# Performance work log

Hardware: AMD Instinct MI355X
Metric: run time of the kernel (lower is better)

The kernel has to match this reference:

```python
import jax, jax.numpy as jnp
import numpy as np
from jax import lax

N_WAY, N_SUPPORT, N_QUERY = 16, 256, 512
D_IN, D_EMB = 4096, 1024
N_CLUSTERS, MAX_ITER = 5, 100


def setup_inputs() -> dict:
    key = jax.random.key(0)
    k1, k2, kw, kb = jax.random.split(key, 4)
    support = jax.random.normal(k1, (N_WAY, N_SUPPORT, D_IN), jnp.float32)
    query = jax.random.normal(k2, (N_WAY, N_QUERY, D_IN), jnp.float32)
    W = jax.random.normal(kw, (D_IN, D_EMB), jnp.float32) / np.float32(np.sqrt(D_IN))
    b = jax.random.normal(kb, (D_EMB,), jnp.float32) * 0.01
    return {"support": support, "query": query, "W": W, "b": b}


def _sqdist(x, c):
    # x [n,d], c [k,d] -> [n,k] squared euclidean distances
    return (jnp.sum(x * x, -1, keepdims=True)
            - 2.0 * (x @ c.T)
            + jnp.sum(c * c, -1))


def _kmeans(x, init):
    # x [n,d], init [k,d]; fixed-iteration Lloyd's kmeans (converged state is a
    # fixed point of the update, matching the torch early-break semantics).
    n = x.shape[0]
    ones = jnp.ones((n,), x.dtype)

    def step(c, _):
        assign = jnp.argmin(_sqdist(x, c), axis=1)              # [n]
        sums = jax.ops.segment_sum(x, assign, num_segments=N_CLUSTERS)
        cnt = jax.ops.segment_sum(ones, assign, num_segments=N_CLUSTERS)
        # empty cluster keeps its old centroid
        new_c = jnp.where(cnt[:, None] > 0,
                          sums / jnp.maximum(cnt, 1.0)[:, None], c)
        return new_c, None

    c, _ = lax.scan(step, init, None, length=MAX_ITER)
    return c


def _forward(support, query, W, b):
    # encoder: shared linear over flattened (n_way * n) rows
    s = (support.reshape(-1, D_IN) @ W + b).reshape(N_WAY, N_SUPPORT, D_EMB)
    q = (query.reshape(-1, D_IN) @ W + b).reshape(N_WAY, N_QUERY, D_EMB)

    # per-class kmeans init: random subset of that class's support embeddings
    keys = jax.random.split(jax.random.key(42), N_WAY)

    def init_fn(key, class_emb):
        idx = jax.random.permutation(key, N_SUPPORT)[:N_CLUSTERS]
        return class_emb[idx]

    inits = jax.vmap(init_fn)(keys, s)                 # [n_way, k, d]
    cluster_protos = jax.vmap(_kmeans)(s, inits)       # [n_way, k, d]
    class_protos = cluster_protos.mean(axis=1)         # [n_way, d]

    # cdist(query_emb [b,n,d], protos [c,d]) -> [b,n,c]
    d2 = (jnp.sum(q * q, -1)[..., None]
          - 2.0 * jnp.einsum('bnd,cd->bnc', q, class_protos)
          + jnp.sum(class_protos * class_protos, -1))
    distances = jnp.sqrt(jnp.maximum(d2, 0.0))
    return -distances                                  # logits [n_way, n_query, n_classes]


def reference(support, query, W, b):
    return _forward(support, query, W, b)
```

## Files before the change

### kernel.cpp

```cpp
#include <hip/hip_runtime.h>
#include <cstdint>
#include <cstddef>


typedef __attribute__((ext_vector_type(4))) float f32x4;
typedef __attribute__((ext_vector_type(8))) short s16x8;
typedef __attribute__((ext_vector_type(4))) short s16x4;
typedef __attribute__((ext_vector_type(8))) __bf16 bf16x8;

__device__ __forceinline__ unsigned short f2bf(float f) {
  unsigned u = __float_as_uint(f);
  return (unsigned short)((u + 0x7FFFu + ((u >> 16) & 1u)) >> 16);
}
__device__ __forceinline__ float bf2f(unsigned short h) {
  return __uint_as_float(((unsigned)h) << 16);
}

typedef const __attribute__((address_space(1))) void GV;
typedef __attribute__((address_space(3))) void LV;
__device__ __forceinline__ void gload_lds16(const void* g, void* l) {
  __builtin_amdgcn_global_load_lds((GV*)g, (LV*)l, 16, 0, 0);
}
__device__ __forceinline__ f32x4 mfma16(bf16x8 a, bf16x8 b, f32x4 c) {
  return __builtin_amdgcn_mfma_f32_16x16x32_bf16(a, b, c, 0, 0, 0);
}
__device__ __forceinline__ float wave_sum(float v) {
#pragma unroll
  for (int st = 1; st < 64; st <<= 1) v += __shfl_xor(v, st);
  return v;
}

__device__ __forceinline__ void tf2x32(unsigned k0, unsigned k1, unsigned x0,
                                       unsigned x1, unsigned& y0, unsigned& y1) {
  unsigned ks0 = k0, ks1 = k1, ks2 = k0 ^ k1 ^ 0x1BD11BDAu;
  x0 += ks0; x1 += ks1;
  const int rA[4] = {13, 15, 26, 6};
  const int rB[4] = {17, 29, 16, 24};
#define ROTL(v, d) (((v) << (d)) | ((v) >> (32 - (d))))
#define RG(R)                                     \
  _Pragma("unroll") for (int i = 0; i < 4; i++) { \
    x0 += x1; x1 = ROTL(x1, R[i]); x1 ^= x0;      \
  }
  RG(rA); x0 += ks1; x1 += ks2 + 1u;
  RG(rB); x0 += ks2; x1 += ks0 + 2u;
  RG(rA); x0 += ks0; x1 += ks1 + 3u;
  RG(rB); x0 += ks1; x1 += ks2 + 4u;
  RG(rA); x0 += ks2; x1 += ks0 + 5u;
#undef RG
#undef ROTL
  y0 = x0; y1 = x1;
}

__global__ __launch_bounds__(256) void prep_k(
    const float* __restrict__ W, const float* __restrict__ sup,
    const float* __restrict__ qry, short* __restrict__ WhiT,
    short* __restrict__ WloT, short* __restrict__ Shi,
    short* __restrict__ Slo, short* __restrict__ Qhi) {
  __shared__ float tile[64][65];
  int t = threadIdx.x;
  if (blockIdx.x < 1024) {
    int bk = blockIdx.x & 63, bn = blockIdx.x >> 6;
#pragma unroll
    for (int i = 0; i < 4; i++) {
      int row = i * 16 + (t >> 4);
      int col = (t & 15) * 4;
      f32x4 v =
          *(const f32x4*)(W + (size_t)(bk * 64 + row) * 1024 + bn * 64 + col);
      tile[row][col + 0] = v[0]; tile[row][col + 1] = v[1];
      tile[row][col + 2] = v[2]; tile[row][col + 3] = v[3];
    }
    __syncthreads();
#pragma unroll
    for (int i = 0; i < 4; i++) {
      int nrow = i * 16 + (t >> 4);
      int kcol = (t & 15) * 4;
      s16x4 hv, lv;
#pragma unroll
      for (int e = 0; e < 4; e++) {
        float v = tile[kcol + e][nrow];
        unsigned short h = f2bf(v);
        hv[e] = (short)h;
        lv[e] = (short)f2bf(v - bf2f(h));
      }
      size_t off = (size_t)(bn * 64 + nrow) * 4096 + bk * 64 + kcol;
      *(s16x4*)(WhiT + off) = hv;
      *(s16x4*)(WloT + off) = lv;
    }
  } else {
    size_t gid = (size_t)(blockIdx.x - 1024) * 256 + t;
    const size_t sup_n8 = (size_t)4096 * 4096 / 8;
    if (gid < sup_n8) {
      const float* src = sup + gid * 8;
      f32x4 v0 = *(const f32x4*)src, v1 = *(const f32x4*)(src + 4);
      s16x8 h, l;
#pragma unroll
      for (int e = 0; e < 4; e++) {
        unsigned short hh = f2bf(v0[e]);
        h[e] = (short)hh; l[e] = (short)f2bf(v0[e] - bf2f(hh));
      }
#pragma unroll
      for (int e = 0; e < 4; e++) {
        unsigned short hh = f2bf(v1[e]);
        h[4 + e] = (short)hh; l[4 + e] = (short)f2bf(v1[e] - bf2f(hh));
      }
      *(s16x8*)(Shi + gid * 8) = h;
      *(s16x8*)(Slo + gid * 8) = l;
    } else {
      size_t q = gid - sup_n8;
      const float* src = qry + q * 8;
      f32x4 v0 = *(const f32x4*)src, v1 = *(const f32x4*)(src + 4);
      s16x8 h;
#pragma unroll
      for (int e = 0; e < 4; e++) h[e] = (short)f2bf(v0[e]);
#pragma unroll
      for (int e = 0; e < 4; e++) h[4 + e] = (short)f2bf(v1[e]);
      *(s16x8*)(Qhi + q * 8) = h;
    }
  }
}

__global__ __launch_bounds__(256) void gemm_sup_k(
    const short* __restrict__ Shi, const short* __restrict__ Slo,
    const short* __restrict__ WhiT, const short* __restrict__ WloT,
    const float* __restrict__ bias, float* __restrict__ emb) {
  __shared__ short lds[24576];
  short* Ah = lds;
  short* Al = lds + 4096;
  short* Bh = lds + 8192;
  short* Bl = lds + 16384;
  const int bid = blockIdx.x;
  const int bm = bid & 63, bn = bid >> 6;
  const int t = threadIdx.x, lane = t & 63, w = t >> 6;
  const int wr = w >> 1, wc = w & 1;
  const int fr = lane & 15, kg = lane >> 4;
  const int ls = lane >> 3, lc = lane & 7;
  const short* Ag = Shi + (size_t)bm * 64 * 4096;
  const short* Alg = Slo + (size_t)bm * 64 * 4096;
  f32x4 acc[2][4] = {};

  for (int kt = 0; kt < 64; ++kt) {
    const int k0 = kt * 64;
    __syncthreads();
    const int cch = (lc ^ ls) * 8;
#pragma unroll
    for (int j = 0; j < 2; j++) {
      int rowl = w * 16 + j * 8 + ls;
      size_t aoff = (size_t)rowl * 4096 + k0 + cch;
      int ldst = (w * 16 + j * 8) * 64;
      gload_lds16(Ag + aoff, Ah + ldst);
      gload_lds16(Alg + aoff, Al + ldst);
    }
#pragma unroll
    for (int j = 0; j < 4; j++) {
      int rowl = w * 32 + j * 8 + ls;
      size_t boff = (size_t)(bn * 128 + rowl) * 4096 + k0 + cch;
      int ldst = (w * 32 + j * 8) * 64;
      gload_lds16(WhiT + boff, Bh + ldst);
      gload_lds16(WloT + boff, Bl + ldst);
    }
    __syncthreads();
#pragma unroll
    for (int ks = 0; ks < 2; ++ks) {
      const int cx = ((ks * 4 + kg) ^ (fr & 7)) * 8;
      bf16x8 ahf[2], alf[2], bhf[4], blf[4];
#pragma unroll
      for (int mi = 0; mi < 2; mi++) {
        int arow = wr * 32 + mi * 16 + fr;
        ahf[mi] = __builtin_bit_cast(bf16x8, *(const s16x8*)(Ah + arow * 64 + cx));
        alf[mi] = __builtin_bit_cast(bf16x8, *(const s16x8*)(Al + arow * 64 + cx));
      }
#pragma unroll
      for (int ni = 0; ni < 4; ni++) {
        int brow = wc * 64 + ni * 16 + fr;
        bhf[ni] = __builtin_bit_cast(bf16x8, *(const s16x8*)(Bh + brow * 64 + cx));
        blf[ni] = __builtin_bit_cast(bf16x8, *(const s16x8*)(Bl + brow * 64 + cx));
      }
#pragma unroll
      for (int mi = 0; mi < 2; mi++)
#pragma unroll
        for (int ni = 0; ni < 4; ni++) {
          acc[mi][ni] = mfma16(ahf[mi], bhf[ni], acc[mi][ni]);
          acc[mi][ni] = mfma16(ahf[mi], blf[ni], acc[mi][ni]);
          acc[mi][ni] = mfma16(alf[mi], bhf[ni], acc[mi][ni]);
        }
    }
  }
#pragma unroll
  for (int ni = 0; ni < 4; ni++) {
    int gc = bn * 128 + wc * 64 + ni * 16 + fr;
    float bv = bias[gc];
#pragma unroll
    for (int mi = 0; mi < 2; mi++) {
      int gr = bm * 64 + wr * 32 + mi * 16 + kg * 4;
#pragma unroll
      for (int r = 0; r < 4; r++)
        emb[(size_t)(gr + r) * 1024 + gc] = acc[mi][ni][r] + bv;
    }
  }
}

__global__ __launch_bounds__(256) void gemm_qry_k(
    const short* __restrict__ Qhi, const short* __restrict__ WhiT,
    const float* __restrict__ bias, float* __restrict__ emb) {
  __shared__ short lds[16384];
  short* Ah = lds;
  short* Bh = lds + 8192;
  const int bid = blockIdx.x;
  const int bm = bid & 63, bn = bid >> 6;
  const int t = threadIdx.x, lane = t & 63, w = t >> 6;
  const int wr = w >> 1, wc = w & 1;
  const int fr = lane & 15, kg = lane >> 4;
  const int ls = lane >> 3, lc = lane & 7;
  const short* Ag = Qhi + (size_t)bm * 128 * 4096;
  f32x4 acc[4][4] = {};

  for (int kt = 0; kt < 64; ++kt) {
    const int k0 = kt * 64;
    __syncthreads();
    const int cch = (lc ^ ls) * 8;
#pragma unroll
    for (int j = 0; j < 4; j++) {
      int rowl = w * 32 + j * 8 + ls;
      size_t aoff = (size_t)rowl * 4096 + k0 + cch;
      size_t boff = (size_t)(bn * 128 + rowl) * 4096 + k0 + cch;
      int ldst = (w * 32 + j * 8) * 64;
      gload_lds16(Ag + aoff, Ah + ldst);
      gload_lds16(WhiT + boff, Bh + ldst);
    }
    __syncthreads();
#pragma unroll
    for (int ks = 0; ks < 2; ++ks) {
      const int cx = ((ks * 4 + kg) ^ (fr & 7)) * 8;
      bf16x8 ahf[4], bhf[4];
#pragma unroll
      for (int mi = 0; mi < 4; mi++) {
        int arow = wr * 64 + mi * 16 + fr;
        ahf[mi] = __builtin_bit_cast(bf16x8, *(const s16x8*)(Ah + arow * 64 + cx));
      }
#pragma unroll
      for (int ni = 0; ni < 4; ni++) {
        int brow = wc * 64 + ni * 16 + fr;
        bhf[ni] = __builtin_bit_cast(bf16x8, *(const s16x8*)(Bh + brow * 64 + cx));
      }
#pragma unroll
      for (int mi = 0; mi < 4; mi++)
#pragma unroll
        for (int ni = 0; ni < 4; ni++)
          acc[mi][ni] = mfma16(ahf[mi], bhf[ni], acc[mi][ni]);
    }
  }
#pragma unroll
  for (int ni = 0; ni < 4; ni++) {
    int gc = bn * 128 + wc * 64 + ni * 16 + fr;
    float bv = bias[gc];
#pragma unroll
    for (int mi = 0; mi < 4; mi++) {
      int gr = 4096 + bm * 128 + wr * 64 + mi * 16 + kg * 4;
#pragma unroll
      for (int r = 0; r < 4; r++)
        emb[(size_t)(gr + r) * 1024 + gc] = acc[mi][ni][r] + bv;
    }
  }
}

__global__ __launch_bounds__(256) void gemm_all_k(
    const float* __restrict__ sup, const float* __restrict__ qry,
    const short* __restrict__ WhiT, const short* __restrict__ WloT,
    const float* __restrict__ bias, float* __restrict__ emb) {
  __shared__ short lds[4 * 128 * 64];
  short* Ah = lds;
  short* Al = lds + 8192;
  short* Bh = lds + 16384;
  short* Bl = lds + 24576;
  const int bid = blockIdx.x;
  const int bm = bid % 96, bn = bid / 96;
  const bool is_sup = bm < 32;
  const int t = threadIdx.x, lane = t & 63, w = t >> 6;
  const int wr = w >> 1, wc = w & 1;
  const int fr = lane & 15, kg = lane >> 4;
  const float* Abase = is_sup ? (sup + (size_t)bm * 128 * 4096)
                              : (qry + (size_t)(bm - 32) * 128 * 4096);
  f32x4 acc[4][4] = {};
  const int ls = lane >> 3, lc = lane & 7;

  for (int kt = 0; kt < 64; ++kt) {
    const int k0 = kt * 64;
    __syncthreads();
#pragma unroll
    for (int i = 0; i < 4; i++) {
      int row = i * 32 + w * 8 + ls;
      const float* src = Abase + (size_t)row * 4096 + k0 + lc * 8;
      f32x4 v0 = *(const f32x4*)src;
      f32x4 v1 = *(const f32x4*)(src + 4);
      s16x8 hs;
#pragma unroll
      for (int e = 0; e < 4; e++) hs[e] = (short)f2bf(v0[e]);
#pragma unroll
      for (int e = 0; e < 4; e++) hs[4 + e] = (short)f2bf(v1[e]);
      int chunk = lc ^ (row & 7);
      *(s16x8*)(Ah + row * 64 + chunk * 8) = hs;
      if (is_sup) {
        s16x8 lsv;
#pragma unroll
        for (int e = 0; e < 4; e++)
          lsv[e] = (short)f2bf(v0[e] - bf2f((unsigned short)hs[e]));
#pragma unroll
        for (int e = 0; e < 4; e++)
          lsv[4 + e] = (short)f2bf(v1[e] - bf2f((unsigned short)hs[4 + e]));
        *(s16x8*)(Al + row * 64 + chunk * 8) = lsv;
      }
    }
#pragma unroll
    for (int j = 0; j < 4; j++) {
      int rowl = w * 32 + j * 8 + ls;
      int cch = (lc ^ (ls & 7)) * 8;
      size_t goff = (size_t)(bn * 128 + rowl) * 4096 + k0 + cch;
      gload_lds16(WhiT + goff, Bh + (w * 32 + j * 8) * 64);
      if (is_sup) gload_lds16(WloT + goff, Bl + (w * 32 + j * 8) * 64);
    }
    __syncthreads();
#pragma unroll
    for (int ks = 0; ks < 2; ++ks) {
      const int cx = ((ks * 4 + kg) ^ (fr & 7)) * 8;
      bf16x8 ahf[4], bhf[4];
#pragma unroll
      for (int mi = 0; mi < 4; mi++) {
        int arow = wr * 64 + mi * 16 + fr;
        ahf[mi] = __builtin_bit_cast(bf16x8, *(const s16x8*)(Ah + arow * 64 + cx));
      }
#pragma unroll
      for (int ni = 0; ni < 4; ni++) {
        int brow = wc * 64 + ni * 16 + fr;
        bhf[ni] = __builtin_bit_cast(bf16x8, *(const s16x8*)(Bh + brow * 64 + cx));
      }
      if (is_sup) {
        bf16x8 alf[4], blf[4];
#pragma unroll
        for (int mi = 0; mi < 4; mi++) {
          int arow = wr * 64 + mi * 16 + fr;
          alf[mi] =
              __builtin_bit_cast(bf16x8, *(const s16x8*)(Al + arow * 64 + cx));
        }
#pragma unroll
        for (int ni = 0; ni < 4; ni++) {
          int brow = wc * 64 + ni * 16 + fr;
          blf[ni] =
              __builtin_bit_cast(bf16x8, *(const s16x8*)(Bl + brow * 64 + cx));
        }
#pragma unroll
        for (int mi = 0; mi < 4; mi++)
#pragma unroll
          for (int ni = 0; ni < 4; ni++) {
            acc[mi][ni] = mfma16(ahf[mi], bhf[ni], acc[mi][ni]);
            acc[mi][ni] = mfma16(ahf[mi], blf[ni], acc[mi][ni]);
            acc[mi][ni] = mfma16(alf[mi], bhf[ni], acc[mi][ni]);
          }
      } else {
#pragma unroll
        for (int mi = 0; mi < 4; mi++)
#pragma unroll
          for (int ni = 0; ni < 4; ni++)
            acc[mi][ni] = mfma16(ahf[mi], bhf[ni], acc[mi][ni]);
      }
    }
  }
#pragma unroll
  for (int ni = 0; ni < 4; ni++) {
    int gc = bn * 128 + wc * 64 + ni * 16 + fr;
    float bv = bias[gc];
#pragma unroll
    for (int mi = 0; mi < 4; mi++) {
      int gr = bm * 128 + wr * 64 + mi * 16 + kg * 4;
#pragma unroll
      for (int r = 0; r < 4; r++)
        emb[(size_t)(gr + r) * 1024 + gc] = acc[mi][ni][r] + bv;
    }
  }
}

__global__ __launch_bounds__(256) void gram_k(const float* __restrict__ emb,
                                              float* __restrict__ G) {
  int c = blockIdx.x >> 4, tl = blockIdx.x & 15, ti = tl >> 2, tj = tl & 3;
  __shared__ float As[64][36];
  __shared__ float Bs[32][68];
  int t = threadIdx.x, ty = t >> 4, tx = t & 15;
  const float* base = emb + (size_t)c * 256 * 1024;
  float acc[4][4] = {};
  for (int k0 = 0; k0 < 1024; k0 += 32) {
    __syncthreads();
    {
      int r = t >> 2, seg = t & 3;
      const float* pa = base + (size_t)(ti * 64 + r) * 1024 + k0 + seg * 8;
      f32x4 va0 = *(const f32x4*)pa, va1 = *(const f32x4*)(pa + 4);
      *(f32x4*)(&As[r][seg * 8]) = va0;
      *(f32x4*)(&As[r][seg * 8 + 4]) = va1;
      const float* pb = base + (size_t)(tj * 64 + r) * 1024 + k0 + seg * 8;
      f32x4 vb0 = *(const f32x4*)pb, vb1 = *(const f32x4*)(pb + 4);
#pragma unroll
      for (int e = 0; e < 4; e++) Bs[seg * 8 + e][r] = vb0[e];
#pragma unroll
      for (int e = 0; e < 4; e++) Bs[seg * 8 + 4 + e][r] = vb1[e];
    }
    __syncthreads();
#pragma unroll 4
    for (int kk = 0; kk < 32; kk++) {
      float a0 = As[ty * 4 + 0][kk], a1 = As[ty * 4 + 1][kk];
      float a2 = As[ty * 4 + 2][kk], a3 = As[ty * 4 + 3][kk];
      f32x4 bv = *(const f32x4*)(&Bs[kk][tx * 4]);
#pragma unroll
      for (int jdx = 0; jdx < 4; jdx++) {
        acc[0][jdx] = fmaf(a0, bv[jdx], acc[0][jdx]);
        acc[1][jdx] = fmaf(a1, bv[jdx], acc[1][jdx]);
        acc[2][jdx] = fmaf(a2, bv[jdx], acc[2][jdx]);
        acc[3][jdx] = fmaf(a3, bv[jdx], acc[3][jdx]);
      }
    }
  }
#pragma unroll
  for (int i = 0; i < 4; i++) {
    int gr = ti * 64 + ty * 4 + i;
#pragma unroll
    for (int j = 0; j < 4; j++)
      G[(size_t)c * 65536 + (size_t)gr * 256 + tj * 64 + tx * 4 + j] = acc[i][j];
  }
}

__global__ __launch_bounds__(256) void diag_k(const float* __restrict__ emb,
                                              float* __restrict__ G) {
  int r = blockIdx.x * 4 + (threadIdx.x >> 6);
  int lane = threadIdx.x & 63;
  const float* x = emb + (size_t)r * 1024;
  double acc = 0.0;
#pragma unroll
  for (int ch = 0; ch < 16; ch++) {
    float v = x[ch * 64 + lane];
    acc = fma((double)v, (double)v, acc);
  }
#pragma unroll
  for (int st = 1; st < 64; st <<= 1) acc += __shfl_xor(acc, st);
  if (lane == 0) {
    int c = r >> 8, i = r & 255;
    G[(size_t)c * 65536 + (size_t)i * 256 + i] = (float)acc;
  }
}

__global__ __launch_bounds__(256) void kmeans2_k(const float* __restrict__ G,
                                                 float* __restrict__ wts) {
  const int c = blockIdx.x;
  const int t = threadIdx.x, lane = t & 63, w = t >> 6;
  __shared__ unsigned dmL[256], nmL[256];
  __shared__ unsigned short chg[256];
  __shared__ unsigned sk[256];
  __shared__ unsigned idx5[5];
  __shared__ float Tpart[4][5], Tu[5], C2[5], Minv[5];
  __shared__ int Hp[4][5], Ncnt[5], cntW[4];

  {
    unsigned o0, o1, s0k, s1k, y0, y1;
    tf2x32(0u, 42u, 0u, (unsigned)c, o0, o1);
    tf2x32(o0, o1, 0u, 1u, s0k, s1k);
    tf2x32(s0k, s1k, 0u, (unsigned)t, y0, y1);
    sk[t] = y0 ^ y1;
  }
  __syncthreads();
  {
    unsigned kt_ = sk[t];
    int rank = 0;
    for (int j = 0; j < 256; j++) {
      unsigned kj = sk[j];
      rank += (kj < kt_ || (kj == kt_ && j < t)) ? 1 : 0;
    }
    if (rank < 5) idx5[rank] = (unsigned)t;
  }
  if (t < 5) Minv[t] = 1.0f;
  __syncthreads();

  unsigned m = 0;
#pragma unroll
  for (int k = 0; k < 5; k++) m |= (idx5[k] == (unsigned)t) ? (1u << k) : 0u;

  const float* Gc = G + (size_t)c * 65536;
  float s0 = Gc[(size_t)idx5[0] * 256 + t];
  float s1 = Gc[(size_t)idx5[1] * 256 + t];
  float s2 = Gc[(size_t)idx5[2] * 256 + t];
  float s3 = Gc[(size_t)idx5[3] * 256 + t];
  float s4 = Gc[(size_t)idx5[4] * 256 + t];

  for (int it = 0; it < 100; ++it) {
    float v0 = (m & 1u) ? s0 : 0.0f;
    float v1 = (m & 2u) ? s1 : 0.0f;
    float v2 = (m & 4u) ? s2 : 0.0f;
    float v3 = (m & 8u) ? s3 : 0.0f;
    float v4 = (m & 16u) ? s4 : 0.0f;
#pragma unroll
    for (int st = 1; st < 64; st <<= 1) {
      v0 += __shfl_xor(v0, st); v1 += __shfl_xor(v1, st);
      v2 += __shfl_xor(v2, st); v3 += __shfl_xor(v3, st);
      v4 += __shfl_xor(v4, st);
    }
    if (lane == 0) {
      Tpart[w][0] = v0; Tpart[w][1] = v1; Tpart[w][2] = v2;
      Tpart[w][3] = v3; Tpart[w][4] = v4;
    }
    __syncthreads();
    if (t < 5) {
      float T = Tpart[0][t] + Tpart[1][t] + Tpart[2][t] + Tpart[3][t];
      float iv = Minv[t];
      Tu[t] = T * iv * iv;
      C2[t] = -2.0f * iv;
    }
    __syncthreads();
    float d0 = fmaf(C2[0], s0, Tu[0]);
    float d1 = fmaf(C2[1], s1, Tu[1]);
    float d2 = fmaf(C2[2], s2, Tu[2]);
    float d3 = fmaf(C2[3], s3, Tu[3]);
    float d4 = fmaf(C2[4], s4, Tu[4]);
    int a_t = 0;
    float dmn = d0;
    if (d1 < dmn) { dmn = d1; a_t = 1; }
    if (d2 < dmn) { dmn = d2; a_t = 2; }
    if (d3 < dmn) { dmn = d3; a_t = 3; }
    if (d4 < dmn) { dmn = d4; a_t = 4; }
#pragma unroll
    for (int k = 0; k < 5; k++) {
      unsigned long long bal = __ballot(a_t == k);
      if (lane == 0) Hp[w][k] = (int)__popcll(bal);
    }
    __syncthreads();
    if (t < 5) Ncnt[t] = Hp[0][t] + Hp[1][t] + Hp[2][t] + Hp[3][t];
    __syncthreads();
    unsigned nm = 0;
#pragma unroll
    for (int k = 0; k < 5; k++) {
      int bit = (Ncnt[k] > 0) ? (a_t == k ? 1 : 0) : (int)((m >> k) & 1u);
      nm |= ((unsigned)bit) << k;
    }
    unsigned dmb = nm ^ m;
    unsigned long long bal = __ballot(dmb != 0);
    int myrank = (int)__popcll(bal & ((1ull << lane) - 1ull));
    if (lane == 0) cntW[w] = (int)__popcll(bal);
    nmL[t] = nm; dmL[t] = dmb;
    __syncthreads();
    int base = 0, ntot = 0;
#pragma unroll
    for (int ww = 0; ww < 4; ww++) {
      int cw = cntW[ww];
      if (ww < w) base += cw;
      ntot += cw;
    }
    if (ntot == 0) break;
    if (dmb != 0) chg[base + myrank] = (unsigned short)t;
    m = nm;
    if (t < 5 && Ncnt[t] > 0) Minv[t] = 1.0f / (float)Ncnt[t];
    __syncthreads();
    for (int p = 0; p < ntot; p += 4) {
      float g[4]; int jj[4];
#pragma unroll
      for (int q = 0; q < 4; q++) {
        int idx = p + q;
        jj[q] = (idx < ntot) ? (int)chg[idx] : -1;
        g[q] = (jj[q] >= 0) ? Gc[(size_t)jj[q] * 256 + t] : 0.0f;
      }
#pragma unroll
      for (int q = 0; q < 4; q++) {
        if (jj[q] < 0) continue;
        unsigned db = dmL[jj[q]], nb = nmL[jj[q]];
        float gv = g[q];
        if (db & 1u)  s0 += (nb & 1u)  ? gv : -gv;
        if (db & 2u)  s1 += (nb & 2u)  ? gv : -gv;
        if (db & 4u)  s2 += (nb & 4u)  ? gv : -gv;
        if (db & 8u)  s3 += (nb & 8u)  ? gv : -gv;
        if (db & 16u) s4 += (nb & 16u) ? gv : -gv;
      }
    }
    __syncthreads();
  }
  float wv = 0.0f;
#pragma unroll
  for (int k = 0; k < 5; k++)
    if ((m >> k) & 1u) wv += 0.2f * Minv[k];
  wts[c * 256 + t] = wv;
}

__global__ __launch_bounds__(256) void proto1_k(const float* __restrict__ emb,
                                                const float* __restrict__ wts,
                                                float* __restrict__ part) {
  int c = blockIdx.x & 15, seg = blockIdx.x >> 4, t = threadIdx.x;
  __shared__ float wl[16];
  if (t < 16) wl[t] = wts[c * 256 + seg * 16 + t];
  __syncthreads();
  f32x4 acc = {};
  const float* base = emb + (size_t)(c * 256 + seg * 16) * 1024 + t * 4;
#pragma unroll
  for (int j = 0; j < 16; j++) {
    f32x4 v = *(const f32x4*)(base + (size_t)j * 1024);
    float wj = wl[j];
#pragma unroll
    for (int e = 0; e < 4; e++) acc[e] = fmaf(wj, v[e], acc[e]);
  }
  *(f32x4*)(part + ((size_t)seg * 16 + c) * 1024 + t * 4) = acc;
}

__global__ __launch_bounds__(256) void proto2_k(const float* __restrict__ part,
                                                float* __restrict__ protos) {
  int c = blockIdx.x, t = threadIdx.x;
  f32x4 acc = {};
#pragma unroll
  for (int seg = 0; seg < 16; seg++) {
    f32x4 v = *(const f32x4*)(part + ((size_t)seg * 16 + c) * 1024 + t * 4);
#pragma unroll
    for (int e = 0; e < 4; e++) acc[e] += v[e];
  }
  *(f32x4*)(protos + (size_t)c * 1024 + t * 4) = acc;
}

__global__ __launch_bounds__(256) void proto_k(const float* __restrict__ emb,
                                               const float* __restrict__ wts,
                                               float* __restrict__ protos) {
  int c = blockIdx.x, t = threadIdx.x;
  __shared__ float wl[256];
  wl[t] = wts[c * 256 + t];
  __syncthreads();
  f32x4 acc = {};
  const float* base = emb + (size_t)c * 256 * 1024 + t * 4;
  for (int j = 0; j < 256; j++) {
    f32x4 v = *(const f32x4*)(base + (size_t)j * 1024);
    float wj = wl[j];
#pragma unroll
    for (int e = 0; e < 4; e++) acc[e] = fmaf(wj, v[e], acc[e]);
  }
  *(f32x4*)(protos + (size_t)c * 1024 + t * 4) = acc;
}

__global__ __launch_bounds__(256) void dist_k(const float* __restrict__ emb,
                                              const float* __restrict__ protos,
                                              float* __restrict__ out) {
  __shared__ float P[16 * 1024];
  int t = threadIdx.x, lane = t & 63, w = t >> 6;
#pragma unroll
  for (int i = 0; i < 16; i++) {
    int off = i * 1024 + t * 4;
    *(f32x4*)(P + off) = *(const f32x4*)(protos + off);
  }
  __syncthreads();
  float psq_keep = 0.0f;
  for (int p = 0; p < 16; p++) {
    float partial = 0.0f;
#pragma unroll
    for (int ch = 0; ch < 16; ch++) {
      float x = P[p * 1024 + ch * 64 + lane];
      partial = fmaf(x, x, partial);
    }
    partial = wave_sum(partial);
    if (lane == p) psq_keep = partial;
  }
  const float* qbase = emb + (size_t)4096 * 1024;
  int r0 = blockIdx.x * 16 + w * 4;
  for (int ri = 0; ri < 4; ri++) {
    int row = r0 + ri;
    const float* q = qbase + (size_t)row * 1024;
    float qv[16];
#pragma unroll
    for (int ch = 0; ch < 16; ch++) qv[ch] = q[ch * 64 + lane];
    float qsq = 0.0f;
#pragma unroll
    for (int ch = 0; ch < 16; ch++) qsq = fmaf(qv[ch], qv[ch], qsq);
    qsq = wave_sum(qsq);
    float dsel = 0.0f;
    for (int p = 0; p < 16; p++) {
      float dp = 0.0f;
#pragma unroll
      for (int ch = 0; ch < 16; ch++)
        dp = fmaf(qv[ch], P[p * 1024 + ch * 64 + lane], dp);
      dp = wave_sum(dp);
      if (lane == p) dsel = dp;
    }
    if (lane < 16) {
      float d2 = qsq - 2.0f * dsel + psq_keep;
      d2 = fmaxf(d2, 0.0f);
      out[(size_t)row * 16 + lane] = -sqrtf(d2);
    }
  }
}

extern "C" void kernel_launch(void* const* d_in, const int* in_sizes, int n_in,
                              void* d_out, int out_size, void* d_ws,
                              size_t ws_size, hipStream_t stream) {
  const float* sup = (const float*)d_in[0];
  const float* qry = (const float*)d_in[1];
  const float* W = (const float*)d_in[2];
  const float* b = (const float*)d_in[3];
  float* out = (float*)d_out;
  char* ws = (char*)d_ws;
  (void)in_sizes; (void)n_in; (void)out_size;

  const size_t NEED_FAST = 206651392ULL;
  if (ws_size >= NEED_FAST) {
    short* WhiT = (short*)(ws + 0);
    short* WloT = (short*)(ws + 8388608);
    short* Shi = (short*)(ws + 16777216);
    short* Slo = (short*)(ws + 50331648);
    short* Qhi = (short*)(ws + 83886080);
    float* emb = (float*)(ws + 150994944);
    float* G = (float*)(ws + 201326592);
    float* wts = (float*)(ws + 205520896);
    float* protos = (float*)(ws + 205537280);
    float* part = (float*)(ws + 205602816);

    prep_k<<<25600, 256, 0, stream>>>(W, sup, qry, WhiT, WloT, Shi, Slo, Qhi);
    gemm_sup_k<<<512, 256, 0, stream>>>(Shi, Slo, WhiT, WloT, b, emb);
    gemm_qry_k<<<512, 256, 0, stream>>>(Qhi, WhiT, b, emb);
    gram_k<<<256, 256, 0, stream>>>(emb, G);
    diag_k<<<1024, 256, 0, stream>>>(emb, G);
    kmeans2_k<<<16, 256, 0, stream>>>(G, wts);
    proto1_k<<<256, 256, 0, stream>>>(emb, wts, part);
    proto2_k<<<16, 256, 0, stream>>>(part, protos);
    dist_k<<<512, 256, 0, stream>>>(emb, protos, out);
  } else {
    short* WhiT = (short*)(ws + 0);
    short* WloT = (short*)(ws + 8388608);
    float* emb = (float*)(ws + 16777216);
    float* G = (float*)(ws + 67108864);
    float* wts = (float*)(ws + 71303168);
    float* protos = (float*)(ws + 71319552);

    prep_k<<<1024, 256, 0, stream>>>(W, sup, qry, WhiT, WloT, (short*)0,
                                     (short*)0, (short*)0);
    gemm_all_k<<<768, 256, 0, stream>>>(sup, qry, WhiT, WloT, b, emb);
    gram_k<<<256, 256, 0, stream>>>(emb, G);
    diag_k<<<1024, 256, 0, stream>>>(emb, G);
    kmeans2_k<<<16, 256, 0, stream>>>(G, wts);
    proto_k<<<16, 256, 0, stream>>>(emb, wts, protos);
    dist_k<<<512, 256, 0, stream>>>(emb, protos, out);
  }
}
```

Baseline: 444.0 us.

## Run kmeans in a single wavefront, fuse gram and diag, grid-stride prep

The kmeans kernel moves from 256 threads (4 waves) to one 64-lane wavefront per class. Each lane holds 4 points, so all block barriers and LDS exchanges are replaced by wave shuffles and ballots. The initial random selection becomes an iterative shuffle min-reduction instead of an O(n) rank count per thread. Gram and diagonal computation are fused into one launch, with the gram blocks skipping diagonal writes to avoid a race, and prep becomes grid-stride with far fewer blocks. The aim is to cut the serial 100-iteration kmeans latency dominated by __syncthreads and to save launch overhead, at the cost of more per-lane work and register pressure.

```diff
diff --git a/kernel.cpp b/kernel.cpp
--- a/kernel.cpp
+++ b/kernel.cpp
@@ -87,34 +87,38 @@
       *(s16x4*)(WloT + off) = lv;
     }
   } else {
-    size_t gid = (size_t)(blockIdx.x - 1024) * 256 + t;
     const size_t sup_n8 = (size_t)4096 * 4096 / 8;
-    if (gid < sup_n8) {
-      const float* src = sup + gid * 8;
-      f32x4 v0 = *(const f32x4*)src, v1 = *(const f32x4*)(src + 4);
-      s16x8 h, l;
-#pragma unroll
-      for (int e = 0; e < 4; e++) {
-        unsigned short hh = f2bf(v0[e]);
-        h[e] = (short)hh; l[e] = (short)f2bf(v0[e] - bf2f(hh));
-      }
-#pragma unroll
-      for (int e = 0; e < 4; e++) {
-        unsigned short hh = f2bf(v1[e]);
-        h[4 + e] = (short)hh; l[4 + e] = (short)f2bf(v1[e] - bf2f(hh));
-      }
-      *(s16x8*)(Shi + gid * 8) = h;
-      *(s16x8*)(Slo + gid * 8) = l;
-    } else {
-      size_t q = gid - sup_n8;
-      const float* src = qry + q * 8;
-      f32x4 v0 = *(const f32x4*)src, v1 = *(const f32x4*)(src + 4);
-      s16x8 h;
-#pragma unroll
-      for (int e = 0; e < 4; e++) h[e] = (short)f2bf(v0[e]);
-#pragma unroll
-      for (int e = 0; e < 4; e++) h[4 + e] = (short)f2bf(v1[e]);
-      *(s16x8*)(Qhi + q * 8) = h;
+    const size_t tot_n8 = sup_n8 + (size_t)8192 * 4096 / 8;
+    size_t stride = (size_t)(gridDim.x - 1024) * 256;
+    for (size_t gid = (size_t)(blockIdx.x - 1024) * 256 + t; gid < tot_n8;
+         gid += stride) {
+      if (gid < sup_n8) {
+        const float* src = sup + gid * 8;
+        f32x4 v0 = *(const f32x4*)src, v1 = *(const f32x4*)(src + 4);
+        s16x8 h, l;
+#pragma unroll
+        for (int e = 0; e < 4; e++) {
+          unsigned short hh = f2bf(v0[e]);
+          h[e] = (short)hh; l[e] = (short)f2bf(v0[e] - bf2f(hh));
+        }
+#pragma unroll
+        for (int e = 0; e < 4; e++) {
+          unsigned short hh = f2bf(v1[e]);
+          h[4 + e] = (short)hh; l[4 + e] = (short)f2bf(v1[e] - bf2f(hh));
+        }
+        *(s16x8*)(Shi + gid * 8) = h;
+        *(s16x8*)(Slo + gid * 8) = l;
+      } else {
+        size_t q = gid - sup_n8;
+        const float* src = qry + q * 8;
+        f32x4 v0 = *(const f32x4*)src, v1 = *(const f32x4*)(src + 4);
+        s16x8 h;
+#pragma unroll
+        for (int e = 0; e < 4; e++) h[e] = (short)f2bf(v0[e]);
+#pragma unroll
+        for (int e = 0; e < 4; e++) h[4 + e] = (short)f2bf(v1[e]);
+        *(s16x8*)(Qhi + q * 8) = h;
+      }
     }
   }
 }
@@ -378,208 +382,231 @@
   }
 }
 
-__global__ __launch_bounds__(256) void gram_k(const float* __restrict__ emb,
-                                              float* __restrict__ G) {
-  int c = blockIdx.x >> 4, tl = blockIdx.x & 15, ti = tl >> 2, tj = tl & 3;
-  __shared__ float As[64][36];
-  __shared__ float Bs[32][68];
-  int t = threadIdx.x, ty = t >> 4, tx = t & 15;
-  const float* base = emb + (size_t)c * 256 * 1024;
-  float acc[4][4] = {};
-  for (int k0 = 0; k0 < 1024; k0 += 32) {
-    __syncthreads();
-    {
-      int r = t >> 2, seg = t & 3;
-      const float* pa = base + (size_t)(ti * 64 + r) * 1024 + k0 + seg * 8;
-      f32x4 va0 = *(const f32x4*)pa, va1 = *(const f32x4*)(pa + 4);
-      *(f32x4*)(&As[r][seg * 8]) = va0;
-      *(f32x4*)(&As[r][seg * 8 + 4]) = va1;
-      const float* pb = base + (size_t)(tj * 64 + r) * 1024 + k0 + seg * 8;
-      f32x4 vb0 = *(const f32x4*)pb, vb1 = *(const f32x4*)(pb + 4);
-#pragma unroll
-      for (int e = 0; e < 4; e++) Bs[seg * 8 + e][r] = vb0[e];
-#pragma unroll
-      for (int e = 0; e < 4; e++) Bs[seg * 8 + 4 + e][r] = vb1[e];
-    }
-    __syncthreads();
+__global__ __launch_bounds__(256) void gramdiag_k(const float* __restrict__ emb,
+                                                  float* __restrict__ G) {
+  if (blockIdx.x < 256) {
+    int c = blockIdx.x >> 4, tl = blockIdx.x & 15, ti = tl >> 2, tj = tl & 3;
+    __shared__ float As[64][36];
+    __shared__ float Bs[32][68];
+    int t = threadIdx.x, ty = t >> 4, tx = t & 15;
+    const float* base = emb + (size_t)c * 256 * 1024;
+    float acc[4][4] = {};
+    for (int k0 = 0; k0 < 1024; k0 += 32) {
+      __syncthreads();
+      {
+        int r = t >> 2, seg = t & 3;
+        const float* pa = base + (size_t)(ti * 64 + r) * 1024 + k0 + seg * 8;
+        f32x4 va0 = *(const f32x4*)pa, va1 = *(const f32x4*)(pa + 4);
+        *(f32x4*)(&As[r][seg * 8]) = va0;
+        *(f32x4*)(&As[r][seg * 8 + 4]) = va1;
+        const float* pb = base + (size_t)(tj * 64 + r) * 1024 + k0 + seg * 8;
+        f32x4 vb0 = *(const f32x4*)pb, vb1 = *(const f32x4*)(pb + 4);
+#pragma unroll
+        for (int e = 0; e < 4; e++) Bs[seg * 8 + e][r] = vb0[e];
+#pragma unroll
+        for (int e = 0; e < 4; e++) Bs[seg * 8 + 4 + e][r] = vb1[e];
+      }
+      __syncthreads();
 #pragma unroll 4
-    for (int kk = 0; kk < 32; kk++) {
-      float a0 = As[ty * 4 + 0][kk], a1 = As[ty * 4 + 1][kk];
-      float a2 = As[ty * 4 + 2][kk], a3 = As[ty * 4 + 3][kk];
-      f32x4 bv = *(const f32x4*)(&Bs[kk][tx * 4]);
-#pragma unroll
-      for (int jdx = 0; jdx < 4; jdx++) {
-        acc[0][jdx] = fmaf(a0, bv[jdx], acc[0][jdx]);
-        acc[1][jdx] = fmaf(a1, bv[jdx], acc[1][jdx]);
-        acc[2][jdx] = fmaf(a2, bv[jdx], acc[2][jdx]);
-        acc[3][jdx] = fmaf(a3, bv[jdx], acc[3][jdx]);
-      }
-    }
-  }
-#pragma unroll
-  for (int i = 0; i < 4; i++) {
-    int gr = ti * 64 + ty * 4 + i;
-#pragma unroll
-    for (int j = 0; j < 4; j++)
-      G[(size_t)c * 65536 + (size_t)gr * 256 + tj * 64 + tx * 4 + j] = acc[i][j];
-  }
-}
-
-__global__ __launch_bounds__(256) void diag_k(const float* __restrict__ emb,
-                                              float* __restrict__ G) {
-  int r = blockIdx.x * 4 + (threadIdx.x >> 6);
-  int lane = threadIdx.x & 63;
-  const float* x = emb + (size_t)r * 1024;
-  double acc = 0.0;
-#pragma unroll
-  for (int ch = 0; ch < 16; ch++) {
-    float v = x[ch * 64 + lane];
-    acc = fma((double)v, (double)v, acc);
-  }
-#pragma unroll
-  for (int st = 1; st < 64; st <<= 1) acc += __shfl_xor(acc, st);
-  if (lane == 0) {
-    int c = r >> 8, i = r & 255;
-    G[(size_t)c * 65536 + (size_t)i * 256 + i] = (float)acc;
-  }
-}
-
-__global__ __launch_bounds__(256) void kmeans2_k(const float* __restrict__ G,
-                                                 float* __restrict__ wts) {
+      for (int kk = 0; kk < 32; kk++) {
+        float a0 = As[ty * 4 + 0][kk], a1 = As[ty * 4 + 1][kk];
+        float a2 = As[ty * 4 + 2][kk], a3 = As[ty * 4 + 3][kk];
+        f32x4 bv = *(const f32x4*)(&Bs[kk][tx * 4]);
+#pragma unroll
+        for (int jdx = 0; jdx < 4; jdx++) {
+          acc[0][jdx] = fmaf(a0, bv[jdx], acc[0][jdx]);
+          acc[1][jdx] = fmaf(a1, bv[jdx], acc[1][jdx]);
+          acc[2][jdx] = fmaf(a2, bv[jdx], acc[2][jdx]);
+          acc[3][jdx] = fmaf(a3, bv[jdx], acc[3][jdx]);
+        }
+      }
+    }
+#pragma unroll
+    for (int i = 0; i < 4; i++) {
+      int gr = ti * 64 + ty * 4 + i;
+#pragma unroll
+      for (int j = 0; j < 4; j++) {
+        int gcl = tj * 64 + tx * 4 + j;
+        if (gr != gcl)
+          G[(size_t)c * 65536 + (size_t)gr * 256 + gcl] = acc[i][j];
+      }
+    }
+  } else {
+    int r = (blockIdx.x - 256) * 4 + (threadIdx.x >> 6);
+    int lane = threadIdx.x & 63;
+    const float* x = emb + (size_t)r * 1024;
+    double acc = 0.0;
+#pragma unroll
+    for (int ch = 0; ch < 16; ch++) {
+      float v = x[ch * 64 + lane];
+      acc = fma((double)v, (double)v, acc);
+    }
+#pragma unroll
+    for (int st = 1; st < 64; st <<= 1) acc += __shfl_xor(acc, st);
+    if (lane == 0) {
+      int c = r >> 8, i = r & 255;
+      G[(size_t)c * 65536 + (size_t)i * 256 + i] = (float)acc;
+    }
+  }
+}
+
+#define APPLY1(db, nb, gg, p)                        \
+  if ((db) & 1u)  s[p][0] += ((nb) & 1u)  ? (gg) : -(gg); \
+  if ((db) & 2u)  s[p][1] += ((nb) & 2u)  ? (gg) : -(gg); \
+  if ((db) & 4u)  s[p][2] += ((nb) & 4u)  ? (gg) : -(gg); \
+  if ((db) & 8u)  s[p][3] += ((nb) & 8u)  ? (gg) : -(gg); \
+  if ((db) & 16u) s[p][4] += ((nb) & 16u) ? (gg) : -(gg);
+
+__global__ __launch_bounds__(64) void kmeans3_k(const float* __restrict__ G,
+                                                float* __restrict__ wts) {
   const int c = blockIdx.x;
-  const int t = threadIdx.x, lane = t & 63, w = t >> 6;
-  __shared__ unsigned dmL[256], nmL[256];
-  __shared__ unsigned short chg[256];
-  __shared__ unsigned sk[256];
-  __shared__ unsigned idx5[5];
-  __shared__ float Tpart[4][5], Tu[5], C2[5], Minv[5];
-  __shared__ int Hp[4][5], Ncnt[5], cntW[4];
-
-  {
-    unsigned o0, o1, s0k, s1k, y0, y1;
-    tf2x32(0u, 42u, 0u, (unsigned)c, o0, o1);
-    tf2x32(o0, o1, 0u, 1u, s0k, s1k);
-    tf2x32(s0k, s1k, 0u, (unsigned)t, y0, y1);
-    sk[t] = y0 ^ y1;
-  }
-  __syncthreads();
-  {
-    unsigned kt_ = sk[t];
-    int rank = 0;
-    for (int j = 0; j < 256; j++) {
-      unsigned kj = sk[j];
-      rank += (kj < kt_ || (kj == kt_ && j < t)) ? 1 : 0;
-    }
-    if (rank < 5) idx5[rank] = (unsigned)t;
-  }
-  if (t < 5) Minv[t] = 1.0f;
-  __syncthreads();
-
-  unsigned m = 0;
-#pragma unroll
-  for (int k = 0; k < 5; k++) m |= (idx5[k] == (unsigned)t) ? (1u << k) : 0u;
-
+  const int lane = threadIdx.x;
+  unsigned o0, o1, s0k, s1k;
+  tf2x32(0u, 42u, 0u, (unsigned)c, o0, o1);
+  tf2x32(o0, o1, 0u, 1u, s0k, s1k);
+  unsigned long long key[4];
+#pragma unroll
+  for (int q = 0; q < 4; q++) {
+    unsigned y0, y1;
+    tf2x32(s0k, s1k, 0u, (unsigned)(lane + 64 * q), y0, y1);
+    key[q] = ((unsigned long long)(y0 ^ y1) << 32) | (unsigned)(lane + 64 * q);
+  }
+  int idx5[5];
+#pragma unroll
+  for (int r = 0; r < 5; r++) {
+    unsigned long long mn = key[0];
+#pragma unroll
+    for (int q = 1; q < 4; q++) mn = key[q] < mn ? key[q] : mn;
+#pragma unroll
+    for (int st = 1; st < 64; st <<= 1) {
+      unsigned long long o = __shfl_xor(mn, st);
+      mn = o < mn ? o : mn;
+    }
+    int widx = (int)(unsigned)(mn & 0xffffffffu);
+    idx5[r] = widx;
+#pragma unroll
+    for (int q = 0; q < 4; q++)
+      if (widx == lane + 64 * q) key[q] = ~0ull;
+  }
+  unsigned m[4];
+#pragma unroll
+  for (int q = 0; q < 4; q++) {
+    unsigned mm = 0;
+#pragma unroll
+    for (int k = 0; k < 5; k++)
+      if (idx5[k] == lane + 64 * q) mm |= 1u << k;
+    m[q] = mm;
+  }
   const float* Gc = G + (size_t)c * 65536;
-  float s0 = Gc[(size_t)idx5[0] * 256 + t];
-  float s1 = Gc[(size_t)idx5[1] * 256 + t];
-  float s2 = Gc[(size_t)idx5[2] * 256 + t];
-  float s3 = Gc[(size_t)idx5[3] * 256 + t];
-  float s4 = Gc[(size_t)idx5[4] * 256 + t];
+  float s[4][5];
+#pragma unroll
+  for (int k = 0; k < 5; k++) {
+    const float* row = Gc + (size_t)idx5[k] * 256;
+#pragma unroll
+    for (int q = 0; q < 4; q++) s[q][k] = row[lane + 64 * q];
+  }
+  float Minv[5] = {1.0f, 1.0f, 1.0f, 1.0f, 1.0f};
 
   for (int it = 0; it < 100; ++it) {
-    float v0 = (m & 1u) ? s0 : 0.0f;
-    float v1 = (m & 2u) ? s1 : 0.0f;
-    float v2 = (m & 4u) ? s2 : 0.0f;
-    float v3 = (m & 8u) ? s3 : 0.0f;
-    float v4 = (m & 16u) ? s4 : 0.0f;
-#pragma unroll
-    for (int st = 1; st < 64; st <<= 1) {
-      v0 += __shfl_xor(v0, st); v1 += __shfl_xor(v1, st);
-      v2 += __shfl_xor(v2, st); v3 += __shfl_xor(v3, st);
-      v4 += __shfl_xor(v4, st);
-    }
-    if (lane == 0) {
-      Tpart[w][0] = v0; Tpart[w][1] = v1; Tpart[w][2] = v2;
-      Tpart[w][3] = v3; Tpart[w][4] = v4;
-    }
-    __syncthreads();
-    if (t < 5) {
-      float T = Tpart[0][t] + Tpart[1][t] + Tpart[2][t] + Tpart[3][t];
-      float iv = Minv[t];
-      Tu[t] = T * iv * iv;
-      C2[t] = -2.0f * iv;
-    }
-    __syncthreads();
-    float d0 = fmaf(C2[0], s0, Tu[0]);
-    float d1 = fmaf(C2[1], s1, Tu[1]);
-    float d2 = fmaf(C2[2], s2, Tu[2]);
-    float d3 = fmaf(C2[3], s3, Tu[3]);
-    float d4 = fmaf(C2[4], s4, Tu[4]);
-    int a_t = 0;
-    float dmn = d0;
-    if (d1 < dmn) { dmn = d1; a_t = 1; }
-    if (d2 < dmn) { dmn = d2; a_t = 2; }
-    if (d3 < dmn) { dmn = d3; a_t = 3; }
-    if (d4 < dmn) { dmn = d4; a_t = 4; }
+    float Tu[5], C2[5];
 #pragma unroll
     for (int k = 0; k < 5; k++) {
-      unsigned long long bal = __ballot(a_t == k);
-      if (lane == 0) Hp[w][k] = (int)__popcll(bal);
-    }
-    __syncthreads();
-    if (t < 5) Ncnt[t] = Hp[0][t] + Hp[1][t] + Hp[2][t] + Hp[3][t];
-    __syncthreads();
-    unsigned nm = 0;
+      float v = 0.0f;
+#pragma unroll
+      for (int q = 0; q < 4; q++)
+        v += ((m[q] >> k) & 1u) ? s[q][k] : 0.0f;
+#pragma unroll
+      for (int st = 1; st < 64; st <<= 1) v += __shfl_xor(v, st);
+      float iv = Minv[k];
+      Tu[k] = v * iv * iv;
+      C2[k] = -2.0f * iv;
+    }
+    int a[4];
+#pragma unroll
+    for (int q = 0; q < 4; q++) {
+      float d0 = fmaf(C2[0], s[q][0], Tu[0]);
+      float d1 = fmaf(C2[1], s[q][1], Tu[1]);
+      float d2 = fmaf(C2[2], s[q][2], Tu[2]);
+      float d3 = fmaf(C2[3], s[q][3], Tu[3]);
+      float d4 = fmaf(C2[4], s[q][4], Tu[4]);
+      int at = 0;
+      float dmn = d0;
+      if (d1 < dmn) { dmn = d1; at = 1; }
+      if (d2 < dmn) { dmn = d2; at = 2; }
+      if (d3 < dmn) { dmn = d3; at = 3; }
+      if (d4 < dmn) { dmn = d4; at = 4; }
+      a[q] = at;
+    }
+    int cnt[5];
 #pragma unroll
     for (int k = 0; k < 5; k++) {
-      int bit = (Ncnt[k] > 0) ? (a_t == k ? 1 : 0) : (int)((m >> k) & 1u);
-      nm |= ((unsigned)bit) << k;
-    }
-    unsigned dmb = nm ^ m;
-    unsigned long long bal = __ballot(dmb != 0);
-    int myrank = (int)__popcll(bal & ((1ull << lane) - 1ull));
-    if (lane == 0) cntW[w] = (int)__popcll(bal);
-    nmL[t] = nm; dmL[t] = dmb;
-    __syncthreads();
-    int base = 0, ntot = 0;
-#pragma unroll
-    for (int ww = 0; ww < 4; ww++) {
-      int cw = cntW[ww];
-      if (ww < w) base += cw;
-      ntot += cw;
-    }
-    if (ntot == 0) break;
-    if (dmb != 0) chg[base + myrank] = (unsigned short)t;
-    m = nm;
-    if (t < 5 && Ncnt[t] > 0) Minv[t] = 1.0f / (float)Ncnt[t];
-    __syncthreads();
-    for (int p = 0; p < ntot; p += 4) {
-      float g[4]; int jj[4];
-#pragma unroll
-      for (int q = 0; q < 4; q++) {
-        int idx = p + q;
-        jj[q] = (idx < ntot) ? (int)chg[idx] : -1;
-        g[q] = (jj[q] >= 0) ? Gc[(size_t)jj[q] * 256 + t] : 0.0f;
-      }
-#pragma unroll
-      for (int q = 0; q < 4; q++) {
-        if (jj[q] < 0) continue;
-        unsigned db = dmL[jj[q]], nb = nmL[jj[q]];
-        float gv = g[q];
-        if (db & 1u)  s0 += (nb & 1u)  ? gv : -gv;
-        if (db & 2u)  s1 += (nb & 2u)  ? gv : -gv;
-        if (db & 4u)  s2 += (nb & 4u)  ? gv : -gv;
-        if (db & 8u)  s3 += (nb & 8u)  ? gv : -gv;
-        if (db & 16u) s4 += (nb & 16u) ? gv : -gv;
-      }
-    }
-    __syncthreads();
-  }
-  float wv = 0.0f;
-#pragma unroll
-  for (int k = 0; k < 5; k++)
-    if ((m >> k) & 1u) wv += 0.2f * Minv[k];
-  wts[c * 256 + t] = wv;
+      int v = (a[0] == k) + (a[1] == k) + (a[2] == k) + (a[3] == k);
+#pragma unroll
+      for (int st = 1; st < 64; st <<= 1) v += __shfl_xor(v, st);
+      cnt[k] = v;
+    }
+    unsigned nm[4], dm[4];
+#pragma unroll
+    for (int q = 0; q < 4; q++) {
+      unsigned nv = 0;
+#pragma unroll
+      for (int k = 0; k < 5; k++) {
+        int bit = (cnt[k] > 0) ? (a[q] == k ? 1 : 0) : (int)((m[q] >> k) & 1u);
+        nv |= ((unsigned)bit) << k;
+      }
+      nm[q] = nv;
+      dm[q] = nv ^ m[q];
+    }
+    unsigned long long bal[4];
+#pragma unroll
+    for (int q = 0; q < 4; q++) bal[q] = __ballot(dm[q] != 0);
+    if ((bal[0] | bal[1] | bal[2] | bal[3]) == 0) break;
+#pragma unroll
+    for (int q = 0; q < 4; q++) m[q] = nm[q];
+#pragma unroll
+    for (int k = 0; k < 5; k++)
+      if (cnt[k] > 0) Minv[k] = 1.0f / (float)cnt[k];
+#pragma unroll
+    for (int q = 0; q < 4; q++) {
+      unsigned long long mask = bal[q];
+      while (mask) {
+#define GATHER(i)                                                      \
+        int j##i = -1;                                                 \
+        unsigned d##i = 0, e##i = 0;                                   \
+        float g##i##0 = 0, g##i##1 = 0, g##i##2 = 0, g##i##3 = 0;      \
+        if (mask) {                                                    \
+          j##i = __builtin_ctzll(mask);                                \
+          mask &= mask - 1;                                            \
+          d##i = __shfl(dm[q], j##i);                                  \
+          e##i = __shfl(nm[q], j##i);                                  \
+          const float* row = Gc + (size_t)(q * 64 + j##i) * 256 + lane;\
+          g##i##0 = row[0];  g##i##1 = row[64];                        \
+          g##i##2 = row[128]; g##i##3 = row[192];                      \
+        }
+        GATHER(0) GATHER(1) GATHER(2) GATHER(3)
+        GATHER(4) GATHER(5) GATHER(6) GATHER(7)
+#undef GATHER
+#define DOAPPLY(i)                        \
+        if (j##i >= 0) {                  \
+          APPLY1(d##i, e##i, g##i##0, 0)  \
+          APPLY1(d##i, e##i, g##i##1, 1)  \
+          APPLY1(d##i, e##i, g##i##2, 2)  \
+          APPLY1(d##i, e##i, g##i##3, 3)  \
+        }
+        DOAPPLY(0) DOAPPLY(1) DOAPPLY(2) DOAPPLY(3)
+        DOAPPLY(4) DOAPPLY(5) DOAPPLY(6) DOAPPLY(7)
+#undef DOAPPLY
+      }
+    }
+  }
+#pragma unroll
+  for (int q = 0; q < 4; q++) {
+    float wv = 0.0f;
+#pragma unroll
+    for (int k = 0; k < 5; k++)
+      if ((m[q] >> k) & 1u) wv += 0.2f * Minv[k];
+    wts[c * 256 + lane + 64 * q] = wv;
+  }
 }
 
 __global__ __launch_bounds__(256) void proto1_k(const float* __restrict__ emb,
@@ -707,12 +734,11 @@
     float* protos = (float*)(ws + 205537280);
     float* part = (float*)(ws + 205602816);
 
-    prep_k<<<25600, 256, 0, stream>>>(W, sup, qry, WhiT, WloT, Shi, Slo, Qhi);
+    prep_k<<<3072, 256, 0, stream>>>(W, sup, qry, WhiT, WloT, Shi, Slo, Qhi);
     gemm_sup_k<<<512, 256, 0, stream>>>(Shi, Slo, WhiT, WloT, b, emb);
     gemm_qry_k<<<512, 256, 0, stream>>>(Qhi, WhiT, b, emb);
-    gram_k<<<256, 256, 0, stream>>>(emb, G);
-    diag_k<<<1024, 256, 0, stream>>>(emb, G);
-    kmeans2_k<<<16, 256, 0, stream>>>(G, wts);
+    gramdiag_k<<<1280, 256, 0, stream>>>(emb, G);
+    kmeans3_k<<<16, 64, 0, stream>>>(G, wts);
     proto1_k<<<256, 256, 0, stream>>>(emb, wts, part);
     proto2_k<<<16, 256, 0, stream>>>(part, protos);
     dist_k<<<512, 256, 0, stream>>>(emb, protos, out);
@@ -727,9 +753,8 @@
     prep_k<<<1024, 256, 0, stream>>>(W, sup, qry, WhiT, WloT, (short*)0,
                                      (short*)0, (short*)0);
     gemm_all_k<<<768, 256, 0, stream>>>(sup, qry, WhiT, WloT, b, emb);
-    gram_k<<<256, 256, 0, stream>>>(emb, G);
-    diag_k<<<1024, 256, 0, stream>>>(emb, G);
-    kmeans2_k<<<16, 256, 0, stream>>>(G, wts);
+    gramdiag_k<<<1280, 256, 0, stream>>>(emb, G);
+    kmeans3_k<<<16, 64, 0, stream>>>(G, wts);
     proto_k<<<16, 256, 0, stream>>>(emb, wts, protos);
     dist_k<<<512, 256, 0, stream>>>(emb, protos, out);
   }
```

New measurement: 452.5 us. No clear change (+1.9%).
